# Optimization experiments

Measured on AMD Instinct MI355X. Metric: run time of the kernel, lower is better.

Reference implementation:

```python
import jax, jax.numpy as jnp
import numpy as np

N_NODES = 100000
N_EDGES = 1600000
IN_DIM = 3
LATENT = 128
LATENT_DEC = 128
NUM_LAYER = 2      # shared-weight middle GCN layers
NUM_LAYER_DEC = 2  # shared-weight middle decoder layers


def _glorot(key, shape):
    fan_in, fan_out = shape[0], shape[1]
    lim = np.sqrt(6.0 / (fan_in + fan_out)).astype(np.float32)
    return jax.random.uniform(key, shape, jnp.float32, -lim, lim)


def setup_inputs() -> dict:
    key = jax.random.key(0)
    ks = jax.random.split(key, 10)
    x = jax.random.normal(ks[0], (N_NODES, IN_DIM), jnp.float32)
    edge_index = jax.random.randint(ks[1], (2, N_EDGES), 0, N_NODES, jnp.int64)
    return {
        "x": x,
        "edge_index": edge_index,
        "W_s": _glorot(ks[2], (IN_DIM, LATENT)),   "b_s": jnp.zeros((LATENT,), jnp.float32),
        "W_m": _glorot(ks[3], (LATENT, LATENT)),   "b_m": jnp.zeros((LATENT,), jnp.float32),
        "W_e": _glorot(ks[4], (LATENT, LATENT)),   "b_e": jnp.zeros((LATENT,), jnp.float32),
        "W_sd": _glorot(ks[5], (LATENT, LATENT_DEC)),    "b_sd": jnp.zeros((LATENT_DEC,), jnp.float32),
        "W_md": _glorot(ks[6], (LATENT_DEC, LATENT_DEC)),"b_md": jnp.zeros((LATENT_DEC,), jnp.float32),
        "W_ed": _glorot(ks[7], (LATENT_DEC, IN_DIM)),    "b_ed": jnp.zeros((IN_DIM,), jnp.float32),
    }


def _gcn_conv(h, W, b, src, dst, dinv):
    # PyG GCNConv: out_i = sum_j norm_ij * (x_j @ W) + b, norm = d^-1/2_i d^-1/2_j
    h = h @ W
    norm = dinv[src] * dinv[dst]                       # [E+N]
    msg = norm[:, None] * h[src]                       # gather + scale
    out = jax.ops.segment_sum(msg, dst, num_segments=N_NODES)  # scatter-add
    return out + b


def reference(x, edge_index, W_s, b_s, W_m, b_m, W_e, b_e, W_sd, b_sd, W_md, b_md, W_ed, b_ed):
    loops = jnp.arange(N_NODES, dtype=edge_index.dtype)
    src = jnp.concatenate([edge_index[0], loops])      # add self-loops
    dst = jnp.concatenate([edge_index[1], loops])
    deg = jax.ops.segment_sum(jnp.ones(src.shape[0], x.dtype), dst, num_segments=N_NODES)
    dinv = jnp.where(deg > 0, jax.lax.rsqrt(deg), 0.0)

    h = jax.nn.relu(_gcn_conv(x, W_s, b_s, src, dst, dinv))
    for _ in range(NUM_LAYER):  # shared weights (ModuleList([layer]*n))
        h = jax.nn.relu(_gcn_conv(h, W_m, b_m, src, dst, dinv))
    h = jax.nn.relu(_gcn_conv(h, W_e, b_e, src, dst, dinv))

    h = jax.nn.relu(h @ W_sd + b_sd)
    for _ in range(NUM_LAYER_DEC):  # shared weights
        h = jax.nn.relu(h @ W_md + b_md)
    y = h @ W_ed + b_ed
    return y + x
```

## Files before the change

### kernel.cpp

```cpp
#include <hip/hip_runtime.h>


typedef __attribute__((ext_vector_type(8))) short short8;
typedef __attribute__((ext_vector_type(4))) float floatx4;
typedef __attribute__((ext_vector_type(2))) float floatx2;

#define BIN_CH 8192
#define NBMAX 512

__device__ __forceinline__ unsigned short f2bf(float f) {
    unsigned int u = __float_as_uint(f);
    u += 0x7fffu + ((u >> 16) & 1u);
    return (unsigned short)(u >> 16);
}
__device__ __forceinline__ unsigned int pk_bf(float a, float b) {
    return (unsigned int)f2bf(a) | ((unsigned int)f2bf(b) << 16);
}
__device__ __forceinline__ float bflo(unsigned int u) { return __uint_as_float(u << 16); }
__device__ __forceinline__ float bfhi(unsigned int u) { return __uint_as_float(u & 0xffff0000u); }
__device__ __forceinline__ unsigned char f2fp8(float f) {
    return (unsigned char)(__builtin_amdgcn_cvt_pk_fp8_f32(f, f, 0, false) & 0xFF);
}


__global__ void pack_kernel(const float* __restrict__ W0, const float* __restrict__ W1,
                            const float* __restrict__ W2, const float* __restrict__ W3,
                            unsigned short* __restrict__ P0, unsigned short* __restrict__ P1,
                            unsigned short* __restrict__ P2, unsigned short* __restrict__ P3,
                            int* __restrict__ gfill, unsigned char* __restrict__ t8zrow,
                            int NB) {
    if (blockIdx.x == 0) {
        for (int i = threadIdx.x; i < NB; i += 256) gfill[i] = 0;
        if (threadIdx.x < 32) ((unsigned int*)t8zrow)[threadIdx.x] = 0;
    }
    int which = blockIdx.x >> 3;
    const float* W = which == 0 ? W0 : which == 1 ? W1 : which == 2 ? W2 : W3;
    unsigned short* P = which == 0 ? P0 : which == 1 ? P1 : which == 2 ? P2 : P3;
    int f = (blockIdx.x & 7) * 256 + threadIdx.x;
    int lane = f & 63, nt = (f >> 6) & 7, kc = f >> 9;
    int kbase = kc * 32 + (lane >> 4) * 8;
    int ncol = nt * 16 + (lane & 15);
    short8 frag;
    #pragma unroll
    for (int j = 0; j < 8; ++j)
        frag[j] = (short)f2bf(W[(size_t)(kbase + j) * 128 + ncol]);
    *((short8*)(P + (size_t)f * 8)) = frag;
}


__global__ __launch_bounds__(512) void bin_kernel(
        const int* __restrict__ src, const int* __restrict__ dst,
        int* __restrict__ gfill, unsigned int* __restrict__ binbuf,
        int NB, int C, int E) {
    __shared__ int hist[NBMAX];
    __shared__ int start[NBMAX];
    __shared__ int dstoff[NBMAX];
    int tid = threadIdx.x;
    int e0 = blockIdx.x * BIN_CH;
    for (int i = tid; i < NB; i += 512) hist[i] = 0;
    __syncthreads();
    for (int i = tid; i < BIN_CH; i += 512) {
        int e = e0 + i;
        if (e < E) atomicAdd(&hist[dst[e] >> 9], 1);
    }
    __syncthreads();
    if (tid < 64) {
        int carry = 0;
        for (int base = 0; base < NB; base += 64) {
            int idx = base + tid;
            int v = (idx < NB) ? hist[idx] : 0;
            int s = v;
            #pragma unroll
            for (int off = 1; off < 64; off <<= 1) {
                int u = __shfl_up(s, off);
                if (tid >= off) s += u;
            }
            if (idx < NB) start[idx] = carry + s - v;
            carry += __shfl(s, 63);
        }
    }
    __syncthreads();
    for (int i = tid; i < NB; i += 512) {
        int cnt = hist[i];
        int g = cnt ? atomicAdd(&gfill[i], cnt) : 0;
        dstoff[i] = g - start[i];
        hist[i] = start[i];
    }
    __syncthreads();
    for (int i = tid; i < BIN_CH; i += 512) {
        int e = e0 + i;
        if (e >= E) continue;
        int d = dst[e];
        int b = d >> 9;
        int slot = atomicAdd(&hist[b], 1);
        int gidx = b * C + dstoff[b] + slot;
        if (gidx < (b + 1) * C)
            binbuf[gidx] = (unsigned int)src[e] | ((unsigned int)(d & 511) << 17);
    }
}

__global__ __launch_bounds__(256) void build_kernel(
        const unsigned int* __restrict__ binbuf, const int* __restrict__ gfill,
        int* __restrict__ rowptr, float* __restrict__ dinv, int* __restrict__ col,
        int NB, int C, int N, int E) {
    __shared__ int h[512];
    __shared__ int hs[512];
    __shared__ int bbase_s;
    int b = blockIdx.x, tid = threadIdx.x;
    int cnt = gfill[b];
    const unsigned int* p = binbuf + (size_t)b * C;
    for (int i = tid; i < 512; i += 256) h[i] = 0;
    __syncthreads();
    if (tid >= 64 && tid < 128) {
        int l = tid - 64;
        int s = 0;
        for (int i = l; i < b; i += 64) s += gfill[i];
        #pragma unroll
        for (int off = 32; off > 0; off >>= 1) s += __shfl_down(s, off);
        if (l == 0) bbase_s = s;
    }
    for (int i = tid; i < cnt; i += 256) atomicAdd(&h[p[i] >> 17], 1);
    __syncthreads();
    if (tid < 64) {
        int carry = 0;
        for (int base = 0; base < 512; base += 64) {
            int v = h[base + tid];
            int s = v;
            #pragma unroll
            for (int off = 1; off < 64; off <<= 1) {
                int u = __shfl_up(s, off);
                if (tid >= off) s += u;
            }
            hs[base + tid] = carry + s - v;
            carry += __shfl(s, 63);
        }
    }
    __syncthreads();
    int base = bbase_s;
    for (int i = tid; i < 512; i += 256) {
        int node = b * 512 + i;
        if (node < N) {
            rowptr[node] = base + hs[i];
            dinv[node] = 1.0f / sqrtf((float)(h[i] + 1));
        }
    }
    if (b == 0 && tid == 0) rowptr[N] = E;
    __syncthreads();
    for (int i = tid; i < cnt; i += 256) {
        unsigned int u = p[i];
        int local = u >> 17;
        int pos = atomicAdd(&hs[local], 1);
        col[base + pos] = (int)(u & 0x1FFFFu);
    }
}


__global__ void in_gemm_kernel(const float* __restrict__ x, const float* __restrict__ W,
                               const float* __restrict__ dinv,
                               unsigned char* __restrict__ t8, int n) {
    int g = blockIdx.x * 256 + threadIdx.x;
    int i = g >> 6, c2 = g & 63;
    if (i >= n) return;
    float x0 = x[i * 3], x1 = x[i * 3 + 1], x2 = x[i * 3 + 2];
    float d = dinv[i];
    int c = c2 * 2;
    float v0 = d * (x0 * W[c]     + x1 * W[128 + c]     + x2 * W[256 + c]);
    float v1 = d * (x0 * W[c + 1] + x1 * W[128 + c + 1] + x2 * W[256 + c + 1]);
    unsigned int pk = __builtin_amdgcn_cvt_pk_fp8_f32(v0, v1, 0, false);
    ((unsigned short*)t8)[(size_t)i * 64 + c2] = (unsigned short)(pk & 0xFFFF);
}


__global__ __launch_bounds__(256) void agg_kernel(
        const unsigned char* __restrict__ t8, const int* __restrict__ rowptr,
        const int* __restrict__ col, const float* __restrict__ dinv,
        const float* __restrict__ bias, unsigned short* __restrict__ out, int n) {
    int node = blockIdx.x * 16 + (threadIdx.x >> 4);
    int lane = threadIdx.x & 63;
    int q16 = lane >> 4;
    int lq  = lane & 15;
    int oct = (lane >> 3) & 1;
    int l8  = lane & 7;
    if (node >= n) node = n - 1;
    floatx2 acc[8];
    #pragma unroll
    for (int i = 0; i < 8; ++i) acc[i] = (floatx2){0.f, 0.f};

    int beg = rowptr[node];
    int deg = rowptr[node + 1] - beg;
    for (int base = 0; base < deg; base += 32) {
        int m = deg - base;
        int jv0 = (lq < m)      ? col[beg + base + lq]      : n;
        int jv1 = (lq + 16 < m) ? col[beg + base + 16 + lq] : n;
        uint4 v[16];
        #pragma unroll
        for (int q = 0; q < 8; ++q) {
            int j = __shfl(jv0, q16 * 16 + q * 2 + oct);
            v[q] = ((const uint4*)(t8 + (size_t)j * 128))[l8];
        }
        #pragma unroll
        for (int q = 0; q < 8; ++q) {
            int j = __shfl(jv1, q16 * 16 + q * 2 + oct);
            v[8 + q] = ((const uint4*)(t8 + (size_t)j * 128))[l8];
        }
        #pragma unroll
        for (int q = 0; q < 16; ++q) {
            acc[0] += __builtin_amdgcn_cvt_pk_f32_fp8(v[q].x, false);
            acc[1] += __builtin_amdgcn_cvt_pk_f32_fp8(v[q].x, true);
            acc[2] += __builtin_amdgcn_cvt_pk_f32_fp8(v[q].y, false);
            acc[3] += __builtin_amdgcn_cvt_pk_f32_fp8(v[q].y, true);
            acc[4] += __builtin_amdgcn_cvt_pk_f32_fp8(v[q].z, false);
            acc[5] += __builtin_amdgcn_cvt_pk_f32_fp8(v[q].z, true);
            acc[6] += __builtin_amdgcn_cvt_pk_f32_fp8(v[q].w, false);
            acc[7] += __builtin_amdgcn_cvt_pk_f32_fp8(v[q].w, true);
        }
    }
    #pragma unroll
    for (int i = 0; i < 8; ++i) {
        acc[i].x += __shfl_xor(acc[i].x, 8);
        acc[i].y += __shfl_xor(acc[i].y, 8);
    }
    uint4 s = ((const uint4*)(t8 + (size_t)node * 128))[l8];
    acc[0] += __builtin_amdgcn_cvt_pk_f32_fp8(s.x, false);
    acc[1] += __builtin_amdgcn_cvt_pk_f32_fp8(s.x, true);
    acc[2] += __builtin_amdgcn_cvt_pk_f32_fp8(s.y, false);
    acc[3] += __builtin_amdgcn_cvt_pk_f32_fp8(s.y, true);
    acc[4] += __builtin_amdgcn_cvt_pk_f32_fp8(s.z, false);
    acc[5] += __builtin_amdgcn_cvt_pk_f32_fp8(s.z, true);
    acc[6] += __builtin_amdgcn_cvt_pk_f32_fp8(s.w, false);
    acc[7] += __builtin_amdgcn_cvt_pk_f32_fp8(s.w, true);

    float di = dinv[node];
    const float4* b4 = (const float4*)bias;
    float o[16];
    #pragma unroll
    for (int k = 0; k < 4; ++k) {
        float4 bb = b4[l8 * 4 + k];
        o[k*4+0] = fmaxf(di * acc[k*2].x   + bb.x, 0.f);
        o[k*4+1] = fmaxf(di * acc[k*2].y   + bb.y, 0.f);
        o[k*4+2] = fmaxf(di * acc[k*2+1].x + bb.z, 0.f);
        o[k*4+3] = fmaxf(di * acc[k*2+1].y + bb.w, 0.f);
    }
    if (oct == 0) {
        uint4 w0, w1;
        w0.x = pk_bf(o[0],  o[1]);  w0.y = pk_bf(o[2],  o[3]);
        w0.z = pk_bf(o[4],  o[5]);  w0.w = pk_bf(o[6],  o[7]);
        w1.x = pk_bf(o[8],  o[9]);  w1.y = pk_bf(o[10], o[11]);
        w1.z = pk_bf(o[12], o[13]); w1.w = pk_bf(o[14], o[15]);
        ((uint4*)(out + (size_t)node * 128))[l8 * 2]     = w0;
        ((uint4*)(out + (size_t)node * 128))[l8 * 2 + 1] = w1;
    }
}


template <bool ENC>
__global__ __launch_bounds__(256) void gemm_mfma_kernel(
        const unsigned short* __restrict__ A, const unsigned short* __restrict__ Wp,
        const float* __restrict__ bias, const float* __restrict__ dinv,
        void* __restrict__ outp, int n) {
    __shared__ unsigned short Ws[16384];
    int tid = threadIdx.x;
    {
        const int4* s = (const int4*)Wp;
        int4* d = (int4*)Ws;
        #pragma unroll
        for (int i = 0; i < 8; ++i) d[tid + 256 * i] = s[tid + 256 * i];
    }
    int wave = tid >> 6, lane = tid & 63;
    int quad = lane >> 4, mrow = lane & 15;
    int row0 = blockIdx.x * 128 + wave * 32;
    __syncthreads();

    short8 af[2][4];
    #pragma unroll
    for (int t = 0; t < 2; ++t) {
        int arow = row0 + t * 16 + mrow; if (arow >= n) arow = n - 1;
        const unsigned short* abase = A + (size_t)arow * 128 + quad * 8;
        #pragma unroll
        for (int kc = 0; kc < 4; ++kc)
            af[t][kc] = *((const short8*)(abase + kc * 32));
    }

    floatx4 acc[2][8];
    #pragma unroll
    for (int t = 0; t < 2; ++t)
        #pragma unroll
        for (int nt = 0; nt < 8; ++nt) acc[t][nt] = (floatx4){0.f, 0.f, 0.f, 0.f};

    #pragma unroll
    for (int kc = 0; kc < 4; ++kc) {
        #pragma unroll
        for (int nt = 0; nt < 8; ++nt) {
            short8 bf = *((const short8*)(Ws + ((kc * 8 + nt) * 64 + lane) * 8));
            acc[0][nt] = __builtin_amdgcn_mfma_f32_16x16x32_bf16(af[0][kc], bf, acc[0][nt], 0, 0, 0);
            acc[1][nt] = __builtin_amdgcn_mfma_f32_16x16x32_bf16(af[1][kc], bf, acc[1][nt], 0, 0, 0);
        }
    }

    #pragma unroll
    for (int t = 0; t < 2; ++t) {
        int rbase = row0 + t * 16 + quad * 4;
        float dv[4];
        if (ENC) {
            #pragma unroll
            for (int r = 0; r < 4; ++r)
                dv[r] = (rbase + r < n) ? dinv[rbase + r] : 0.f;
        }
        #pragma unroll
        for (int nt = 0; nt < 8; ++nt) {
            int colc = nt * 16 + mrow;
            float bcol = ENC ? 0.f : bias[colc];
            #pragma unroll
            for (int r = 0; r < 4; ++r) {
                int row = rbase + r;
                if (row < n) {
                    float v = acc[t][nt][r];
                    if (ENC) {
                        v *= dv[r];
                        ((unsigned char*)outp)[(size_t)row * 128 + colc] = f2fp8(v);
                    } else {
                        v = fmaxf(v + bcol, 0.f);
                        ((unsigned short*)outp)[(size_t)row * 128 + colc] = f2bf(v);
                    }
                }
            }
        }
    }
}


__global__ __launch_bounds__(256) void gemm_out_kernel(
        const unsigned short* __restrict__ A, const unsigned short* __restrict__ Wp,
        const float* __restrict__ bias, const float* __restrict__ W_ed,
        const float* __restrict__ b_ed, const float* __restrict__ x,
        float* __restrict__ out, int n) {
    __shared__ unsigned short Ws[16384];
    int tid = threadIdx.x;
    {
        const int4* s = (const int4*)Wp;
        int4* d = (int4*)Ws;
        #pragma unroll
        for (int i = 0; i < 8; ++i) d[tid + 256 * i] = s[tid + 256 * i];
    }
    int wave = tid >> 6, lane = tid & 63;
    int quad = lane >> 4, mrow = lane & 15;
    int row0 = blockIdx.x * 128 + wave * 32;
    __syncthreads();

    short8 af[2][4];
    #pragma unroll
    for (int t = 0; t < 2; ++t) {
        int arow = row0 + t * 16 + mrow; if (arow >= n) arow = n - 1;
        const unsigned short* abase = A + (size_t)arow * 128 + quad * 8;
        #pragma unroll
        for (int kc = 0; kc < 4; ++kc)
            af[t][kc] = *((const short8*)(abase + kc * 32));
    }

    floatx4 acc[2][8];
    #pragma unroll
    for (int t = 0; t < 2; ++t)
        #pragma unroll
        for (int nt = 0; nt < 8; ++nt) acc[t][nt] = (floatx4){0.f, 0.f, 0.f, 0.f};

    #pragma unroll
    for (int kc = 0; kc < 4; ++kc) {
        #pragma unroll
        for (int nt = 0; nt < 8; ++nt) {
            short8 bf = *((const short8*)(Ws + ((kc * 8 + nt) * 64 + lane) * 8));
            acc[0][nt] = __builtin_amdgcn_mfma_f32_16x16x32_bf16(af[0][kc], bf, acc[0][nt], 0, 0, 0);
            acc[1][nt] = __builtin_amdgcn_mfma_f32_16x16x32_bf16(af[1][kc], bf, acc[1][nt], 0, 0, 0);
        }
    }

    float wed[8][3];
    #pragma unroll
    for (int nt = 0; nt < 8; ++nt) {
        int c = nt * 16 + mrow;
        #pragma unroll
        for (int k = 0; k < 3; ++k) wed[nt][k] = W_ed[c * 3 + k];
    }
    #pragma unroll
    for (int t = 0; t < 2; ++t) {
        #pragma unroll
        for (int r = 0; r < 4; ++r) {
            float s0 = 0.f, s1 = 0.f, s2 = 0.f;
            #pragma unroll
            for (int nt = 0; nt < 8; ++nt) {
                float v = fmaxf(acc[t][nt][r] + bias[nt * 16 + mrow], 0.f);
                s0 += v * wed[nt][0]; s1 += v * wed[nt][1]; s2 += v * wed[nt][2];
            }
            #pragma unroll
            for (int off = 1; off < 16; off <<= 1) {
                s0 += __shfl_xor(s0, off);
                s1 += __shfl_xor(s1, off);
                s2 += __shfl_xor(s2, off);
            }
            if (mrow == 0) {
                int row = row0 + t * 16 + quad * 4 + r;
                if (row < n) {
                    out[row * 3 + 0] = s0 + b_ed[0] + x[row * 3 + 0];
                    out[row * 3 + 1] = s1 + b_ed[1] + x[row * 3 + 1];
                    out[row * 3 + 2] = s2 + b_ed[2] + x[row * 3 + 2];
                }
            }
        }
    }
}


extern "C" void kernel_launch(void* const* d_in, const int* in_sizes, int n_in,
                              void* d_out, int out_size, void* d_ws, size_t ws_size,
                              hipStream_t stream) {
    const float* x    = (const float*)d_in[0];
    const int*   ei   = (const int*)d_in[1];
    const float* W_s  = (const float*)d_in[2];
    const float* b_s  = (const float*)d_in[3];
    const float* W_m  = (const float*)d_in[4];
    const float* b_m  = (const float*)d_in[5];
    const float* W_e  = (const float*)d_in[6];
    const float* b_e  = (const float*)d_in[7];
    const float* W_sd = (const float*)d_in[8];
    const float* b_sd = (const float*)d_in[9];
    const float* W_md = (const float*)d_in[10];
    const float* b_md = (const float*)d_in[11];
    const float* W_ed = (const float*)d_in[12];
    const float* b_ed = (const float*)d_in[13];
    float* outp = (float*)d_out;

    const int N = in_sizes[0] / 3;
    const int E = in_sizes[1] / 2;
    const int* src = ei;
    const int* dst = ei + E;

    const int NB = (N + 511) >> 9;
    const int C  = (((E / NB) * 3 / 2) + 255) & ~255;

    char* p = (char*)d_ws;
    auto carve = [&](size_t bytes) {
        void* r = (void*)p;
        p += (bytes + 255) & ~(size_t)255;
        return r;
    };
    int*   rowptr = (int*)  carve((size_t)(N + 1) * 4);
    int*   col    = (int*)  carve((size_t)E * 4);
    float* dinv   = (float*)carve((size_t)N * 4);
    int*   gfill  = (int*)  carve((size_t)NB * 4);
    unsigned int* binbuf = (unsigned int*)carve((size_t)NB * C * 4);
    unsigned short* Wp_m  = (unsigned short*)carve(16384 * 2);
    unsigned short* Wp_e  = (unsigned short*)carve(16384 * 2);
    unsigned short* Wp_sd = (unsigned short*)carve(16384 * 2);
    unsigned short* Wp_md = (unsigned short*)carve(16384 * 2);
    unsigned char*  T8 = (unsigned char*) carve((size_t)(N + 1) * 128);
    unsigned short* A  = (unsigned short*)carve((size_t)N * 128 * 2);
    unsigned short* Bm = (unsigned short*)carve((size_t)N * 128 * 2);
    (void)ws_size;

    const int gBin = (E + BIN_CH - 1) / BIN_CH;
    const int gNode16 = (N + 15) / 16;
    const int gRow128 = (N + 127) / 128;

    pack_kernel<<<32, 256, 0, stream>>>(W_m, W_e, W_sd, W_md, Wp_m, Wp_e, Wp_sd, Wp_md,
                                        gfill, T8 + (size_t)N * 128, NB);

    bin_kernel<<<gBin, 512, 0, stream>>>(src, dst, gfill, binbuf, NB, C, E);
    build_kernel<<<NB, 256, 0, stream>>>(binbuf, gfill, rowptr, dinv, col, NB, C, N, E);

    in_gemm_kernel<<<(N * 64 + 255) / 256, 256, 0, stream>>>(x, W_s, dinv, T8, N);
    agg_kernel<<<gNode16, 256, 0, stream>>>(T8, rowptr, col, dinv, b_s, A, N);

    gemm_mfma_kernel<true><<<gRow128, 256, 0, stream>>>(A, Wp_m, nullptr, dinv, T8, N);
    agg_kernel<<<gNode16, 256, 0, stream>>>(T8, rowptr, col, dinv, b_m, A, N);

    gemm_mfma_kernel<true><<<gRow128, 256, 0, stream>>>(A, Wp_m, nullptr, dinv, T8, N);
    agg_kernel<<<gNode16, 256, 0, stream>>>(T8, rowptr, col, dinv, b_m, A, N);

    gemm_mfma_kernel<true><<<gRow128, 256, 0, stream>>>(A, Wp_e, nullptr, dinv, T8, N);
    agg_kernel<<<gNode16, 256, 0, stream>>>(T8, rowptr, col, dinv, b_e, A, N);

    gemm_mfma_kernel<false><<<gRow128, 256, 0, stream>>>(A, Wp_sd, b_sd, nullptr, Bm, N);
    gemm_mfma_kernel<false><<<gRow128, 256, 0, stream>>>(Bm, Wp_md, b_md, nullptr, A, N);
    gemm_out_kernel<<<gRow128, 256, 0, stream>>>(A, Wp_md, b_md, W_ed, b_ed, x, outp, N);
}
```

Measured before the change: 414.2 us.

## Fuse decoder GEMM chain into one kernel and fold input GEMM into build

The three decoder GEMMs (sd, md, md plus the output projection) now run in a single kernel. Intermediate activations stay in padded LDS tiles, and the weights are restaged between layers, so the per-layer HBM round trips of 100k x 128 bf16 activations and two launches go away. The input 3->128 projection is also folded into the end of build_kernel, which computes dinv locally, removing another launch and a dinv reload. The encoder GEMM also now issues its A-fragment loads before the weight-staging barrier. In exchange the decoder uses more LDS per block (about 49 KB), which may lower occupancy, and build_kernel takes on the extra per-node projection work.

```diff
diff --git a/kernel.cpp b/kernel.cpp
--- a/kernel.cpp
+++ b/kernel.cpp
@@ -7,6 +7,7 @@
 
 #define BIN_CH 8192
 #define NBMAX 512
+#define HS_STRIDE 68
 
 __device__ __forceinline__ unsigned short f2bf(float f) {
     unsigned int u = __float_as_uint(f);
@@ -16,10 +17,14 @@
 __device__ __forceinline__ unsigned int pk_bf(float a, float b) {
     return (unsigned int)f2bf(a) | ((unsigned int)f2bf(b) << 16);
 }
-__device__ __forceinline__ float bflo(unsigned int u) { return __uint_as_float(u << 16); }
-__device__ __forceinline__ float bfhi(unsigned int u) { return __uint_as_float(u & 0xffff0000u); }
 __device__ __forceinline__ unsigned char f2fp8(float f) {
     return (unsigned char)(__builtin_amdgcn_cvt_pk_fp8_f32(f, f, 0, false) & 0xFF);
+}
+__device__ __forceinline__ short8 ld_frag(const unsigned short* p) {
+    uint2 a = *(const uint2*)p;
+    uint2 b = *(const uint2*)(p + 4);
+    int4 v = make_int4((int)a.x, (int)a.y, (int)b.x, (int)b.y);
+    return __builtin_bit_cast(short8, v);
 }
 
 
@@ -101,15 +106,18 @@
 
 __global__ __launch_bounds__(256) void build_kernel(
         const unsigned int* __restrict__ binbuf, const int* __restrict__ gfill,
+        const float* __restrict__ x, const float* __restrict__ W_s,
         int* __restrict__ rowptr, float* __restrict__ dinv, int* __restrict__ col,
-        int NB, int C, int N, int E) {
+        unsigned char* __restrict__ t8, int NB, int C, int N, int E) {
     __shared__ int h[512];
     __shared__ int hs[512];
     __shared__ int bbase_s;
+    __shared__ float WsS[384];
     int b = blockIdx.x, tid = threadIdx.x;
     int cnt = gfill[b];
     const unsigned int* p = binbuf + (size_t)b * C;
     for (int i = tid; i < 512; i += 256) h[i] = 0;
+    for (int i = tid; i < 384; i += 256) WsS[i] = W_s[i];
     __syncthreads();
     if (tid >= 64 && tid < 128) {
         int l = tid - 64;
@@ -152,22 +160,18 @@
         int pos = atomicAdd(&hs[local], 1);
         col[base + pos] = (int)(u & 0x1FFFFu);
     }
-}
-
-
-__global__ void in_gemm_kernel(const float* __restrict__ x, const float* __restrict__ W,
-                               const float* __restrict__ dinv,
-                               unsigned char* __restrict__ t8, int n) {
-    int g = blockIdx.x * 256 + threadIdx.x;
-    int i = g >> 6, c2 = g & 63;
-    if (i >= n) return;
-    float x0 = x[i * 3], x1 = x[i * 3 + 1], x2 = x[i * 3 + 2];
-    float d = dinv[i];
-    int c = c2 * 2;
-    float v0 = d * (x0 * W[c]     + x1 * W[128 + c]     + x2 * W[256 + c]);
-    float v1 = d * (x0 * W[c + 1] + x1 * W[128 + c + 1] + x2 * W[256 + c + 1]);
-    unsigned int pk = __builtin_amdgcn_cvt_pk_fp8_f32(v0, v1, 0, false);
-    ((unsigned short*)t8)[(size_t)i * 64 + c2] = (unsigned short)(pk & 0xFFFF);
+    for (int idx = tid; idx < 512 * 64; idx += 256) {
+        int il = idx >> 6, c2 = idx & 63;
+        int node = b * 512 + il;
+        if (node >= N) continue;
+        float d = 1.0f / sqrtf((float)(h[il] + 1));
+        float x0 = x[node * 3], x1 = x[node * 3 + 1], x2 = x[node * 3 + 2];
+        int c = c2 * 2;
+        float v0 = d * (x0 * WsS[c]     + x1 * WsS[128 + c]     + x2 * WsS[256 + c]);
+        float v1 = d * (x0 * WsS[c + 1] + x1 * WsS[128 + c + 1] + x2 * WsS[256 + c + 1]);
+        unsigned int pk = __builtin_amdgcn_cvt_pk_fp8_f32(v0, v1, 0, false);
+        ((unsigned short*)t8)[(size_t)node * 64 + c2] = (unsigned short)(pk & 0xFFFF);
+    }
 }
 
 
@@ -253,40 +257,19 @@
 }
 
 
-template <bool ENC>
-__global__ __launch_bounds__(256) void gemm_mfma_kernel(
-        const unsigned short* __restrict__ A, const unsigned short* __restrict__ Wp,
-        const float* __restrict__ bias, const float* __restrict__ dinv,
-        void* __restrict__ outp, int n) {
-    __shared__ unsigned short Ws[16384];
-    int tid = threadIdx.x;
-    {
-        const int4* s = (const int4*)Wp;
-        int4* d = (int4*)Ws;
-        #pragma unroll
-        for (int i = 0; i < 8; ++i) d[tid + 256 * i] = s[tid + 256 * i];
-    }
-    int wave = tid >> 6, lane = tid & 63;
-    int quad = lane >> 4, mrow = lane & 15;
-    int row0 = blockIdx.x * 128 + wave * 32;
-    __syncthreads();
-
-    short8 af[2][4];
-    #pragma unroll
-    for (int t = 0; t < 2; ++t) {
-        int arow = row0 + t * 16 + mrow; if (arow >= n) arow = n - 1;
-        const unsigned short* abase = A + (size_t)arow * 128 + quad * 8;
-        #pragma unroll
-        for (int kc = 0; kc < 4; ++kc)
-            af[t][kc] = *((const short8*)(abase + kc * 32));
-    }
-
-    floatx4 acc[2][8];
+__device__ __forceinline__ void stage_ws(unsigned short* Ws, const unsigned short* Wp, int tid) {
+    const int4* s = (const int4*)Wp;
+    int4* d = (int4*)Ws;
+    #pragma unroll
+    for (int i = 0; i < 8; ++i) d[tid + 256 * i] = s[tid + 256 * i];
+}
+
+__device__ __forceinline__ void gemm_regs(const short8 af[2][4], const unsigned short* Ws,
+                                          int lane, floatx4 acc[2][8]) {
     #pragma unroll
     for (int t = 0; t < 2; ++t)
         #pragma unroll
         for (int nt = 0; nt < 8; ++nt) acc[t][nt] = (floatx4){0.f, 0.f, 0.f, 0.f};
-
     #pragma unroll
     for (int kc = 0; kc < 4; ++kc) {
         #pragma unroll
@@ -296,56 +279,97 @@
             acc[1][nt] = __builtin_amdgcn_mfma_f32_16x16x32_bf16(af[1][kc], bf, acc[1][nt], 0, 0, 0);
         }
     }
+}
+
+__device__ __forceinline__ void gemm_lds(const unsigned short* Hs, const unsigned short* Ws,
+                                         int wav, int lane, floatx4 acc[2][8]) {
+    int quad = lane >> 4, mrow = lane & 15;
+    short8 af[2][4];
+    #pragma unroll
+    for (int t = 0; t < 2; ++t)
+        #pragma unroll
+        for (int kc = 0; kc < 4; ++kc)
+            af[t][kc] = ld_frag(Hs + (wav * 32 + t * 16 + mrow) * HS_STRIDE + (kc * 4 + quad) * 8);
+    gemm_regs(af, Ws, lane, acc);
+}
+
+__device__ __forceinline__ void relu_store_hs(
+        unsigned short* Hs, const float* __restrict__ bias,
+        floatx4 acc[2][8], int wav, int lane) {
+    int quad = lane >> 4, mrow = lane & 15;
+    #pragma unroll
+    for (int t = 0; t < 2; ++t) {
+        #pragma unroll
+        for (int nt = 0; nt < 8; ++nt) {
+            int colc = nt * 16 + mrow;
+            float bcol = bias[colc];
+            #pragma unroll
+            for (int r = 0; r < 4; ++r) {
+                int rowl = wav * 32 + t * 16 + quad * 4 + r;
+                Hs[rowl * HS_STRIDE + colc] = f2bf(fmaxf(acc[t][nt][r] + bcol, 0.f));
+            }
+        }
+    }
+}
+
+
+__global__ __launch_bounds__(256) void gemm_enc_kernel(
+        const unsigned short* __restrict__ A, const unsigned short* __restrict__ Wp,
+        const float* __restrict__ dinv, unsigned char* __restrict__ outp, int n) {
+    __shared__ unsigned short Ws[16384];
+    int tid = threadIdx.x;
+    stage_ws(Ws, Wp, tid);
+    int wave = tid >> 6, lane = tid & 63;
+    int quad = lane >> 4, mrow = lane & 15;
+    int row0 = blockIdx.x * 128 + wave * 32;
+
+    short8 af[2][4];
+    #pragma unroll
+    for (int t = 0; t < 2; ++t) {
+        int arow = row0 + t * 16 + mrow; if (arow >= n) arow = n - 1;
+        const unsigned short* abase = A + (size_t)arow * 128 + quad * 8;
+        #pragma unroll
+        for (int kc = 0; kc < 4; ++kc)
+            af[t][kc] = *((const short8*)(abase + kc * 32));
+    }
+    __syncthreads();
+    floatx4 acc[2][8];
+    gemm_regs(af, Ws, lane, acc);
 
     #pragma unroll
     for (int t = 0; t < 2; ++t) {
         int rbase = row0 + t * 16 + quad * 4;
         float dv[4];
-        if (ENC) {
-            #pragma unroll
-            for (int r = 0; r < 4; ++r)
-                dv[r] = (rbase + r < n) ? dinv[rbase + r] : 0.f;
-        }
+        #pragma unroll
+        for (int r = 0; r < 4; ++r)
+            dv[r] = (rbase + r < n) ? dinv[rbase + r] : 0.f;
         #pragma unroll
         for (int nt = 0; nt < 8; ++nt) {
             int colc = nt * 16 + mrow;
-            float bcol = ENC ? 0.f : bias[colc];
             #pragma unroll
             for (int r = 0; r < 4; ++r) {
                 int row = rbase + r;
-                if (row < n) {
-                    float v = acc[t][nt][r];
-                    if (ENC) {
-                        v *= dv[r];
-                        ((unsigned char*)outp)[(size_t)row * 128 + colc] = f2fp8(v);
-                    } else {
-                        v = fmaxf(v + bcol, 0.f);
-                        ((unsigned short*)outp)[(size_t)row * 128 + colc] = f2bf(v);
-                    }
-                }
-            }
-        }
-    }
-}
-
-
-__global__ __launch_bounds__(256) void gemm_out_kernel(
-        const unsigned short* __restrict__ A, const unsigned short* __restrict__ Wp,
-        const float* __restrict__ bias, const float* __restrict__ W_ed,
-        const float* __restrict__ b_ed, const float* __restrict__ x,
-        float* __restrict__ out, int n) {
+                if (row < n)
+                    outp[(size_t)row * 128 + colc] = f2fp8(acc[t][nt][r] * dv[r]);
+            }
+        }
+    }
+}
+
+
+__global__ __launch_bounds__(256) void decoder_kernel(
+        const unsigned short* __restrict__ A,
+        const unsigned short* __restrict__ Wp_sd, const float* __restrict__ b_sd,
+        const unsigned short* __restrict__ Wp_md, const float* __restrict__ b_md,
+        const float* __restrict__ W_ed, const float* __restrict__ b_ed,
+        const float* __restrict__ x, float* __restrict__ out, int n) {
     __shared__ unsigned short Ws[16384];
+    __shared__ unsigned short Hs[128 * HS_STRIDE];
     int tid = threadIdx.x;
-    {
-        const int4* s = (const int4*)Wp;
-        int4* d = (int4*)Ws;
-        #pragma unroll
-        for (int i = 0; i < 8; ++i) d[tid + 256 * i] = s[tid + 256 * i];
-    }
-    int wave = tid >> 6, lane = tid & 63;
+    stage_ws(Ws, Wp_sd, tid);
+    int wav = tid >> 6, lane = tid & 63;
     int quad = lane >> 4, mrow = lane & 15;
-    int row0 = blockIdx.x * 128 + wave * 32;
-    __syncthreads();
+    int row0 = blockIdx.x * 128 + wav * 32;
 
     short8 af[2][4];
     #pragma unroll
@@ -356,22 +380,17 @@
         for (int kc = 0; kc < 4; ++kc)
             af[t][kc] = *((const short8*)(abase + kc * 32));
     }
+    __syncthreads();
 
     floatx4 acc[2][8];
-    #pragma unroll
-    for (int t = 0; t < 2; ++t)
-        #pragma unroll
-        for (int nt = 0; nt < 8; ++nt) acc[t][nt] = (floatx4){0.f, 0.f, 0.f, 0.f};
-
-    #pragma unroll
-    for (int kc = 0; kc < 4; ++kc) {
-        #pragma unroll
-        for (int nt = 0; nt < 8; ++nt) {
-            short8 bf = *((const short8*)(Ws + ((kc * 8 + nt) * 64 + lane) * 8));
-            acc[0][nt] = __builtin_amdgcn_mfma_f32_16x16x32_bf16(af[0][kc], bf, acc[0][nt], 0, 0, 0);
-            acc[1][nt] = __builtin_amdgcn_mfma_f32_16x16x32_bf16(af[1][kc], bf, acc[1][nt], 0, 0, 0);
-        }
-    }
+    gemm_regs(af, Ws, lane, acc);
+    relu_store_hs(Hs, b_sd, acc, wav, lane);
+    __syncthreads();
+    stage_ws(Ws, Wp_md, tid);
+    __syncthreads();
+    gemm_lds(Hs, Ws, wav, lane, acc);
+    relu_store_hs(Hs, b_md, acc, wav, lane);
+    gemm_lds(Hs, Ws, wav, lane, acc);
 
     float wed[8][3];
     #pragma unroll
@@ -387,7 +406,7 @@
             float s0 = 0.f, s1 = 0.f, s2 = 0.f;
             #pragma unroll
             for (int nt = 0; nt < 8; ++nt) {
-                float v = fmaxf(acc[t][nt][r] + bias[nt * 16 + mrow], 0.f);
+                float v = fmaxf(acc[t][nt][r] + b_md[nt * 16 + mrow], 0.f);
                 s0 += v * wed[nt][0]; s1 += v * wed[nt][1]; s2 += v * wed[nt][2];
             }
             #pragma unroll
@@ -453,7 +472,6 @@
     unsigned short* Wp_md = (unsigned short*)carve(16384 * 2);
     unsigned char*  T8 = (unsigned char*) carve((size_t)(N + 1) * 128);
     unsigned short* A  = (unsigned short*)carve((size_t)N * 128 * 2);
-    unsigned short* Bm = (unsigned short*)carve((size_t)N * 128 * 2);
     (void)ws_size;
 
     const int gBin = (E + BIN_CH - 1) / BIN_CH;
@@ -464,21 +482,17 @@
                                         gfill, T8 + (size_t)N * 128, NB);
 
     bin_kernel<<<gBin, 512, 0, stream>>>(src, dst, gfill, binbuf, NB, C, E);
-    build_kernel<<<NB, 256, 0, stream>>>(binbuf, gfill, rowptr, dinv, col, NB, C, N, E);
-
-    in_gemm_kernel<<<(N * 64 + 255) / 256, 256, 0, stream>>>(x, W_s, dinv, T8, N);
+    build_kernel<<<NB, 256, 0, stream>>>(binbuf, gfill, x, W_s, rowptr, dinv, col, T8,
+                                         NB, C, N, E);
+
     agg_kernel<<<gNode16, 256, 0, stream>>>(T8, rowptr, col, dinv, b_s, A, N);
-
-    gemm_mfma_kernel<true><<<gRow128, 256, 0, stream>>>(A, Wp_m, nullptr, dinv, T8, N);
+    gemm_enc_kernel<<<gRow128, 256, 0, stream>>>(A, Wp_m, dinv, T8, N);
     agg_kernel<<<gNode16, 256, 0, stream>>>(T8, rowptr, col, dinv, b_m, A, N);
-
-    gemm_mfma_kernel<true><<<gRow128, 256, 0, stream>>>(A, Wp_m, nullptr, dinv, T8, N);
+    gemm_enc_kernel<<<gRow128, 256, 0, stream>>>(A, Wp_m, dinv, T8, N);
     agg_kernel<<<gNode16, 256, 0, stream>>>(T8, rowptr, col, dinv, b_m, A, N);
-
-    gemm_mfma_kernel<true><<<gRow128, 256, 0, stream>>>(A, Wp_e, nullptr, dinv, T8, N);
+    gemm_enc_kernel<<<gRow128, 256, 0, stream>>>(A, Wp_e, dinv, T8, N);
     agg_kernel<<<gNode16, 256, 0, stream>>>(T8, rowptr, col, dinv, b_e, A, N);
 
-    gemm_mfma_kernel<false><<<gRow128, 256, 0, stream>>>(A, Wp_sd, b_sd, nullptr, Bm, N);
-    gemm_mfma_kernel<false><<<gRow128, 256, 0, stream>>>(Bm, Wp_md, b_md, nullptr, A, N);
-    gemm_out_kernel<<<gRow128, 256, 0, stream>>>(A, Wp_md, b_md, W_ed, b_ed, x, outp, N);
-}
+    decoder_kernel<<<gRow128, 256, 0, stream>>>(A, Wp_sd, b_sd, Wp_md, b_md,
+                                                W_ed, b_ed, x, outp, N);
+}
```

Result: no change. 417.1 us (+0.7%).
